# Performance work log

Measured on AMD Instinct MI355X. Metric: run time of the kernel, lower is better.

## Reference

```python
import jax, jax.numpy as jnp
import numpy as np

B, D, L, H = 2048, 64, 64, 512  # batch, in_dim, latent_space, hidden


def setup_inputs() -> dict:
    key = jax.random.key(0)
    ks = jax.random.split(key, 12)
    inp = {
        "x": jax.random.normal(ks[0], (B, D), jnp.float32),
        "koopman": jax.random.normal(ks[1], (B, L, D), jnp.float32),
    }
    dims = [(L, H), (H, H), (H, H), (H, D)]
    k = 2
    for pfx in ("s", "t"):
        for j, (fi, fo) in enumerate(dims):
            inp[f"{pfx}W{j+1}"] = jax.random.normal(ks[k], (fi, fo), jnp.float32) / np.sqrt(fi).astype(np.float32)
            inp[f"{pfx}b{j+1}"] = jnp.zeros((fo,), jnp.float32)
            k += 1
    return inp


def _mlp(z, W1, b1, W2, b2, W3, b3, W4, b4):
    h = jnp.tanh(z @ W1 + b1)
    h = jnp.tanh(h @ W2 + b2)
    h = jnp.tanh(h @ W3 + b3)
    return h @ W4 + b4


def reference(x, koopman,
              sW1, sb1, sW2, sb2, sW3, sb3, sW4, sb4,
              tW1, tb1, tW2, tb2, tW3, tb3, tW4, tb4):
    # koopman: (B, L, D) -> z: (B, D, L); column i of the torch loop is z[:, i, :]
    z = jnp.swapaxes(koopman, 1, 2)
    s = _mlp(z, sW1, sb1, sW2, sb2, sW3, sb3, sW4, sb4)  # (B, D, D)
    t = _mlp(z, tW1, tb1, tW2, tb2, tW3, tb3, tW4, tb4)  # (B, D, D)
    # loop kept only output column i for input column i -> diagonal over last two dims
    ds = jnp.diagonal(s, axis1=1, axis2=2)  # (B, D)
    dt = jnp.diagonal(t, axis1=1, axis2=2)  # (B, D)
    return (x - dt) * jnp.exp(-ds)
```

## Files before the change

kernel.cpp:

```cpp
#include <hip/hip_runtime.h>


typedef _Float16 f16;
typedef _Float16 f16x4 __attribute__((ext_vector_type(4)));
typedef _Float16 f16x8 __attribute__((ext_vector_type(8)));
typedef float f32x16 __attribute__((ext_vector_type(16)));

#define WPACK_PER_NET 589824
#define OFF_W1 0
#define OFF_W2 32768
#define OFF_W3 294912
#define OFF_W4T 557056
#define WPACK_BYTES (2u * WPACK_PER_NET * sizeof(f16))

__global__ void pack_weights(const float* __restrict__ sW1, const float* __restrict__ sW2,
                             const float* __restrict__ sW3, const float* __restrict__ sW4,
                             const float* __restrict__ tW1, const float* __restrict__ tW2,
                             const float* __restrict__ tW3, const float* __restrict__ tW4,
                             f16* __restrict__ dst) {
  int idx8 = (blockIdx.x * 256 + threadIdx.x) * 8;
  if (idx8 >= 2 * WPACK_PER_NET) return;
  int net = idx8 >= WPACK_PER_NET;
  int f = idx8 - net * WPACK_PER_NET;
  const float* W1 = net ? tW1 : sW1;
  const float* W2 = net ? tW2 : sW2;
  const float* W3 = net ? tW3 : sW3;
  const float* W4 = net ? tW4 : sW4;
  f16x8 o;
  if (f < OFF_W2) {
    int lane = (f >> 3) & 63, g = (f >> 9) & 15, ks = f >> 13;
    int r0 = ks * 16 + (lane >> 5) * 8, c = g * 32 + (lane & 31);
#pragma unroll
    for (int j = 0; j < 8; j++) o[j] = (f16)W1[(r0 + j) * 512 + c];
  } else if (f < OFF_W3) {
    int f2 = f - OFF_W2;
    int lane = (f2 >> 3) & 63, g = (f2 >> 9) & 15, ks = f2 >> 13;
    int r0 = ks * 16 + (lane >> 5) * 8, c = g * 32 + (lane & 31);
#pragma unroll
    for (int j = 0; j < 8; j++) o[j] = (f16)W2[(r0 + j) * 512 + c];
  } else if (f < OFF_W4T) {
    int f3 = f - OFF_W3;
    int lane = (f3 >> 3) & 63, g = (f3 >> 9) & 15, ks = f3 >> 13;
    int r0 = ks * 16 + (lane >> 5) * 8, c = g * 32 + (lane & 31);
#pragma unroll
    for (int j = 0; j < 8; j++) o[j] = (f16)W3[(r0 + j) * 512 + c];
  } else {
    int f4 = f - OFF_W4T;
    int i = f4 >> 9, k0 = f4 & 511;
#pragma unroll
    for (int j = 0; j < 8; j++) o[j] = (f16)W4[(k0 + j) * 64 + i];
  }
  *(f16x8*)(dst + net * WPACK_PER_NET + f) = o;
}

__device__ __forceinline__ int zbidx(int k, int j) {
  return ((k >> 4) * 2 + (j >> 5)) * 512 + ((j & 31) + 32 * ((k >> 3) & 1)) * 8 + (k & 7);
}

__device__ __forceinline__ float fast_tanh(float x) {
  float e = __expf(x + x);
  return fmaf(-2.0f, __builtin_amdgcn_rcpf(e + 1.0f), 1.0f);
}

template <bool PACKED>
__device__ __forceinline__ void load_a(const f16* __restrict__ Wblk,
                                       const float* __restrict__ Wraw,
                                       int ks, int wave, int lane, f16x8* adst) {
  if (PACKED) {
#pragma unroll
    for (int it = 0; it < 2; it++)
      adst[it] = *(const f16x8*)(Wblk + ((ks * 16 + wave * 2 + it) * 64 + lane) * 8);
  } else {
    int r0 = ks * 16 + (lane >> 5) * 8;
    int n0 = wave * 64 + (lane & 31);
#pragma unroll
    for (int it = 0; it < 2; it++) {
      f16x8 v;
#pragma unroll
      for (int j = 0; j < 8; j++) v[j] = (f16)Wraw[(r0 + j) * 512 + n0 + it * 32];
      adst[it] = v;
    }
  }
}

template <int NS, bool PACKED, bool ALIASED>
__device__ __forceinline__ void mlp_layer(const f16* __restrict__ Wblk,
                                          const float* __restrict__ Wraw,
                                          const float* __restrict__ bias,
                                          const f16* Bsrc, f16* Tout,
                                          int wave, int lane) {
  f32x16 acc[2][2];
#pragma unroll
  for (int it = 0; it < 2; it++)
#pragma unroll
    for (int jt = 0; jt < 2; jt++)
#pragma unroll
      for (int e = 0; e < 16; e++) acc[it][jt][e] = 0.f;

  f16x8 aw[2][2];
  load_a<PACKED>(Wblk, Wraw, 0, wave, lane, aw[0]);
#pragma unroll
  for (int ks = 0; ks < NS; ks++) {
    if (ks + 1 < NS) load_a<PACKED>(Wblk, Wraw, ks + 1, wave, lane, aw[(ks + 1) & 1]);
    const f16* bb = Bsrc + ks * 1024 + lane * 8;
    f16x8 b0 = *(const f16x8*)bb;
    f16x8 b1 = *(const f16x8*)(bb + 512);
#pragma unroll
    for (int it = 0; it < 2; it++) {
      acc[it][0] = __builtin_amdgcn_mfma_f32_32x32x16_f16(aw[ks & 1][it], b0,
                                                          acc[it][0], 0, 0, 0);
      acc[it][1] = __builtin_amdgcn_mfma_f32_32x32x16_f16(aw[ks & 1][it], b1,
                                                          acc[it][1], 0, 0, 0);
    }
  }

  const int h = lane >> 5;
  f16x4 hv[2][2][4];
#pragma unroll
  for (int it = 0; it < 2; it++)
#pragma unroll
    for (int rq = 0; rq < 4; rq++) {
      float4 bv = *(const float4*)&bias[wave * 64 + it * 32 + rq * 8 + h * 4];
#pragma unroll
      for (int jt = 0; jt < 2; jt++) {
        f16x4 v;
#pragma unroll
        for (int rr = 0; rr < 4; rr++)
          v[rr] = (f16)fast_tanh(acc[it][jt][rq * 4 + rr] + (&bv.x)[rr]);
        hv[it][jt][rq] = v;
      }
    }

  if (ALIASED) __syncthreads();

  f16* wb = Tout + wave * 4096 + (lane & 31) * 8 + 4 * h;
#pragma unroll
  for (int it = 0; it < 2; it++)
#pragma unroll
    for (int jt = 0; jt < 2; jt++)
#pragma unroll
      for (int rq = 0; rq < 4; rq++)
        *(f16x4*)(wb + it * 2048 + jt * 512 + (rq >> 1) * 1024 + (rq & 1) * 256) =
            hv[it][jt][rq];
  __syncthreads();
}

template <bool PACKED>
__global__ __launch_bounds__(512, 4) void decoder_main(
    const float* __restrict__ x, const float* __restrict__ koop,
    const f16* __restrict__ wpack,
    const float* __restrict__ sW1, const float* __restrict__ sW2,
    const float* __restrict__ sW3, const float* __restrict__ sW4,
    const float* __restrict__ tW1, const float* __restrict__ tW2,
    const float* __restrict__ tW3, const float* __restrict__ tW4,
    const float* __restrict__ sb1, const float* __restrict__ sb2,
    const float* __restrict__ sb3, const float* __restrict__ sb4,
    const float* __restrict__ tb1, const float* __restrict__ tb2,
    const float* __restrict__ tb3, const float* __restrict__ tb4,
    float* __restrict__ out) {
  __shared__ __align__(16) f16 ZB[4096];
  __shared__ __align__(16) f16 HA[32768];
  __shared__ float pp[512];
  __shared__ float redBuf[2][64];

  const int b = blockIdx.x;
  const int t = threadIdx.x;
  const int wave = t >> 6, lane = t & 63;

  const float* kb = koop + b * 4096;
#pragma unroll
  for (int i = 0; i < 8; i++) {
    int flat = t + 512 * i;
    ZB[zbidx(flat >> 6, flat & 63)] = (f16)kb[flat];
  }
  __syncthreads();

  for (int net = 0; net < 2; net++) {
    const f16* wb = PACKED ? (wpack + net * WPACK_PER_NET) : (const f16*)0;
    const float* W1 = net ? tW1 : sW1;
    const float* W2 = net ? tW2 : sW2;
    const float* W3 = net ? tW3 : sW3;
    const float* W4 = net ? tW4 : sW4;
    const float* b1 = net ? tb1 : sb1;
    const float* b2 = net ? tb2 : sb2;
    const float* b3 = net ? tb3 : sb3;
    const float* b4 = net ? tb4 : sb4;
    mlp_layer<4, PACKED, false>(PACKED ? wb + OFF_W1 : 0, W1, b1, ZB, HA, wave, lane);
    mlp_layer<32, PACKED, true>(PACKED ? wb + OFF_W2 : 0, W2, b2, HA, HA, wave, lane);
    mlp_layer<32, PACKED, true>(PACKED ? wb + OFF_W3 : 0, W3, b3, HA, HA, wave, lane);

    {
      float p = 0.f;
#pragma unroll
      for (int q = 0; q < 8; q++) {
        int k0 = wave * 64 + q * 8;
        f16x8 hv = *(const f16x8*)&HA[zbidx(k0, lane)];
#pragma unroll
        for (int j = 0; j < 8; j++)
          p += (float)hv[j] * W4[(k0 + j) * 64 + lane];
      }
      pp[wave * 64 + lane] = p;
    }
    __syncthreads();
    if (t < 64) {
      float s = b4[t];
#pragma unroll
      for (int o = 0; o < 8; o++) s += pp[o * 64 + t];
      redBuf[net][t] = s;
    }
    __syncthreads();
  }

  if (t < 64) {
    out[b * 64 + t] = (x[b * 64 + t] - redBuf[1][t]) * __expf(-redBuf[0][t]);
  }
}

extern "C" void kernel_launch(void* const* d_in, const int* in_sizes, int n_in,
                              void* d_out, int out_size, void* d_ws, size_t ws_size,
                              hipStream_t stream) {
  const float* x    = (const float*)d_in[0];
  const float* koop = (const float*)d_in[1];
  const float* sW1 = (const float*)d_in[2];  const float* sb1 = (const float*)d_in[3];
  const float* sW2 = (const float*)d_in[4];  const float* sb2 = (const float*)d_in[5];
  const float* sW3 = (const float*)d_in[6];  const float* sb3 = (const float*)d_in[7];
  const float* sW4 = (const float*)d_in[8];  const float* sb4 = (const float*)d_in[9];
  const float* tW1 = (const float*)d_in[10]; const float* tb1 = (const float*)d_in[11];
  const float* tW2 = (const float*)d_in[12]; const float* tb2 = (const float*)d_in[13];
  const float* tW3 = (const float*)d_in[14]; const float* tb3 = (const float*)d_in[15];
  const float* tW4 = (const float*)d_in[16]; const float* tb4 = (const float*)d_in[17];
  float* out = (float*)d_out;

  if (ws_size >= (size_t)WPACK_BYTES) {
    f16* wpack = (f16*)d_ws;
    pack_weights<<<576, 256, 0, stream>>>(sW1, sW2, sW3, sW4, tW1, tW2, tW3, tW4, wpack);
    decoder_main<true><<<2048, 512, 0, stream>>>(
        x, koop, wpack, sW1, sW2, sW3, sW4, tW1, tW2, tW3, tW4,
        sb1, sb2, sb3, sb4, tb1, tb2, tb3, tb4, out);
  } else {
    decoder_main<false><<<2048, 512, 0, stream>>>(
        x, koop, (const f16*)0, sW1, sW2, sW3, sW4, tW1, tW2, tW3, tW4,
        sb1, sb2, sb3, sb4, tb1, tb2, tb3, tb4, out);
  }
}
```

Before: 468.3 us.

## Fuse layer-3 epilogue with W4 diagonal dot product and prefetch B operands

Layer 3's tanh output is no longer written to shared memory and reread. Each lane instead multiplies its accumulator values directly against the matching W4 row and reduces across half-waves with a shuffle, which removes one LDS round trip and one barrier per network. The K-loop now double-buffers the B fragments read from LDS alongside the A weights and raises wave priority around the MFMA group. W4 packing is dropped from the pre-pass, since W4 is now read directly as fp32 from global memory.

```diff
diff --git a/kernel.cpp b/kernel.cpp
--- a/kernel.cpp
+++ b/kernel.cpp
@@ -10,22 +10,21 @@
 #define OFF_W1 0
 #define OFF_W2 32768
 #define OFF_W3 294912
-#define OFF_W4T 557056
+#define PACK_ELEMS 557056
 #define WPACK_BYTES (2u * WPACK_PER_NET * sizeof(f16))
 
 __global__ void pack_weights(const float* __restrict__ sW1, const float* __restrict__ sW2,
-                             const float* __restrict__ sW3, const float* __restrict__ sW4,
+                             const float* __restrict__ sW3,
                              const float* __restrict__ tW1, const float* __restrict__ tW2,
-                             const float* __restrict__ tW3, const float* __restrict__ tW4,
+                             const float* __restrict__ tW3,
                              f16* __restrict__ dst) {
   int idx8 = (blockIdx.x * 256 + threadIdx.x) * 8;
-  if (idx8 >= 2 * WPACK_PER_NET) return;
-  int net = idx8 >= WPACK_PER_NET;
-  int f = idx8 - net * WPACK_PER_NET;
+  if (idx8 >= 2 * PACK_ELEMS) return;
+  int net = idx8 >= PACK_ELEMS;
+  int f = idx8 - net * PACK_ELEMS;
   const float* W1 = net ? tW1 : sW1;
   const float* W2 = net ? tW2 : sW2;
   const float* W3 = net ? tW3 : sW3;
-  const float* W4 = net ? tW4 : sW4;
   f16x8 o;
   if (f < OFF_W2) {
     int lane = (f >> 3) & 63, g = (f >> 9) & 15, ks = f >> 13;
@@ -38,17 +37,12 @@
     int r0 = ks * 16 + (lane >> 5) * 8, c = g * 32 + (lane & 31);
 #pragma unroll
     for (int j = 0; j < 8; j++) o[j] = (f16)W2[(r0 + j) * 512 + c];
-  } else if (f < OFF_W4T) {
+  } else {
     int f3 = f - OFF_W3;
     int lane = (f3 >> 3) & 63, g = (f3 >> 9) & 15, ks = f3 >> 13;
     int r0 = ks * 16 + (lane >> 5) * 8, c = g * 32 + (lane & 31);
 #pragma unroll
     for (int j = 0; j < 8; j++) o[j] = (f16)W3[(r0 + j) * 512 + c];
-  } else {
-    int f4 = f - OFF_W4T;
-    int i = f4 >> 9, k0 = f4 & 511;
-#pragma unroll
-    for (int j = 0; j < 8; j++) o[j] = (f16)W4[(k0 + j) * 64 + i];
   }
   *(f16x8*)(dst + net * WPACK_PER_NET + f) = o;
 }
@@ -80,6 +74,38 @@
       for (int j = 0; j < 8; j++) v[j] = (f16)Wraw[(r0 + j) * 512 + n0 + it * 32];
       adst[it] = v;
     }
+  }
+}
+
+template <int NS, bool PACKED>
+__device__ __forceinline__ void kloop(const f16* __restrict__ Wblk,
+                                      const float* __restrict__ Wraw,
+                                      const f16* Bsrc, int wave, int lane,
+                                      f32x16 acc[2][2]) {
+  f16x8 aw[2][2], bn[2][2];
+  load_a<PACKED>(Wblk, Wraw, 0, wave, lane, aw[0]);
+  {
+    const f16* bb = Bsrc + lane * 8;
+    bn[0][0] = *(const f16x8*)bb;
+    bn[0][1] = *(const f16x8*)(bb + 512);
+  }
+#pragma unroll
+  for (int ks = 0; ks < NS; ks++) {
+    if (ks + 1 < NS) {
+      load_a<PACKED>(Wblk, Wraw, ks + 1, wave, lane, aw[(ks + 1) & 1]);
+      const f16* bb = Bsrc + (ks + 1) * 1024 + lane * 8;
+      bn[(ks + 1) & 1][0] = *(const f16x8*)bb;
+      bn[(ks + 1) & 1][1] = *(const f16x8*)(bb + 512);
+    }
+    __builtin_amdgcn_s_setprio(1);
+#pragma unroll
+    for (int it = 0; it < 2; it++) {
+      acc[it][0] = __builtin_amdgcn_mfma_f32_32x32x16_f16(
+          aw[ks & 1][it], bn[ks & 1][0], acc[it][0], 0, 0, 0);
+      acc[it][1] = __builtin_amdgcn_mfma_f32_32x32x16_f16(
+          aw[ks & 1][it], bn[ks & 1][1], acc[it][1], 0, 0, 0);
+    }
+    __builtin_amdgcn_s_setprio(0);
   }
 }
 
@@ -97,22 +123,7 @@
 #pragma unroll
       for (int e = 0; e < 16; e++) acc[it][jt][e] = 0.f;
 
-  f16x8 aw[2][2];
-  load_a<PACKED>(Wblk, Wraw, 0, wave, lane, aw[0]);
-#pragma unroll
-  for (int ks = 0; ks < NS; ks++) {
-    if (ks + 1 < NS) load_a<PACKED>(Wblk, Wraw, ks + 1, wave, lane, aw[(ks + 1) & 1]);
-    const f16* bb = Bsrc + ks * 1024 + lane * 8;
-    f16x8 b0 = *(const f16x8*)bb;
-    f16x8 b1 = *(const f16x8*)(bb + 512);
-#pragma unroll
-    for (int it = 0; it < 2; it++) {
-      acc[it][0] = __builtin_amdgcn_mfma_f32_32x32x16_f16(aw[ks & 1][it], b0,
-                                                          acc[it][0], 0, 0, 0);
-      acc[it][1] = __builtin_amdgcn_mfma_f32_32x32x16_f16(aw[ks & 1][it], b1,
-                                                          acc[it][1], 0, 0, 0);
-    }
-  }
+  kloop<NS, PACKED>(Wblk, Wraw, Bsrc, wave, lane, acc);
 
   const int h = lane >> 5;
   f16x4 hv[2][2][4];
@@ -142,6 +153,49 @@
       for (int rq = 0; rq < 4; rq++)
         *(f16x4*)(wb + it * 2048 + jt * 512 + (rq >> 1) * 1024 + (rq & 1) * 256) =
             hv[it][jt][rq];
+  __syncthreads();
+}
+
+template <int NS, bool PACKED>
+__device__ __forceinline__ void l3_diag(const f16* __restrict__ Wblk,
+                                        const float* __restrict__ Wraw,
+                                        const float* __restrict__ b3,
+                                        const float* __restrict__ W4,
+                                        const f16* Bsrc, float* pp,
+                                        int wave, int lane) {
+  f32x16 acc[2][2];
+#pragma unroll
+  for (int it = 0; it < 2; it++)
+#pragma unroll
+    for (int jt = 0; jt < 2; jt++)
+#pragma unroll
+      for (int e = 0; e < 16; e++) acc[it][jt][e] = 0.f;
+
+  kloop<NS, PACKED>(Wblk, Wraw, Bsrc, wave, lane, acc);
+
+  const int h = lane >> 5, dl = lane & 31;
+  float p0 = 0.f, p1 = 0.f;
+#pragma unroll
+  for (int it = 0; it < 2; it++)
+#pragma unroll
+    for (int rq = 0; rq < 4; rq++) {
+      float4 bv = *(const float4*)&b3[wave * 64 + it * 32 + rq * 8 + h * 4];
+#pragma unroll
+      for (int rr = 0; rr < 4; rr++) {
+        int kp = wave * 64 + it * 32 + rq * 8 + h * 4 + rr;
+        const float* wrow = W4 + kp * 64 + dl;
+        float h30 = fast_tanh(acc[it][0][rq * 4 + rr] + (&bv.x)[rr]);
+        float h31 = fast_tanh(acc[it][1][rq * 4 + rr] + (&bv.x)[rr]);
+        p0 = fmaf(h30, wrow[0], p0);
+        p1 = fmaf(h31, wrow[32], p1);
+      }
+    }
+  p0 += __shfl_down(p0, 32);
+  p1 += __shfl_down(p1, 32);
+  if (lane < 32) {
+    pp[wave * 64 + lane] = p0;
+    pp[wave * 64 + 32 + lane] = p1;
+  }
   __syncthreads();
 }
 
@@ -187,21 +241,8 @@
     const float* b4 = net ? tb4 : sb4;
     mlp_layer<4, PACKED, false>(PACKED ? wb + OFF_W1 : 0, W1, b1, ZB, HA, wave, lane);
     mlp_layer<32, PACKED, true>(PACKED ? wb + OFF_W2 : 0, W2, b2, HA, HA, wave, lane);
-    mlp_layer<32, PACKED, true>(PACKED ? wb + OFF_W3 : 0, W3, b3, HA, HA, wave, lane);
-
-    {
-      float p = 0.f;
-#pragma unroll
-      for (int q = 0; q < 8; q++) {
-        int k0 = wave * 64 + q * 8;
-        f16x8 hv = *(const f16x8*)&HA[zbidx(k0, lane)];
-#pragma unroll
-        for (int j = 0; j < 8; j++)
-          p += (float)hv[j] * W4[(k0 + j) * 64 + lane];
-      }
-      pp[wave * 64 + lane] = p;
-    }
-    __syncthreads();
+    l3_diag<32, PACKED>(PACKED ? wb + OFF_W3 : 0, W3, b3, W4, HA, pp, wave, lane);
+
     if (t < 64) {
       float s = b4[t];
 #pragma unroll
@@ -233,7 +274,7 @@
 
   if (ws_size >= (size_t)WPACK_BYTES) {
     f16* wpack = (f16*)d_ws;
-    pack_weights<<<576, 256, 0, stream>>>(sW1, sW2, sW3, sW4, tW1, tW2, tW3, tW4, wpack);
+    pack_weights<<<544, 256, 0, stream>>>(sW1, sW2, sW3, tW1, tW2, tW3, wpack);
     decoder_main<true><<<2048, 512, 0, stream>>>(
         x, koop, wpack, sW1, sW2, sW3, sW4, tW1, tW2, tW3, tW4,
         sb1, sb2, sb3, sb4, tb1, tb2, tb3, tb4, out);
```

After: 454.3 us. -3.0%, faster.
